# Kernel optimization log

Hardware: AMD Instinct MI355X
Metric: run time of the kernel (lower is better)

## Reference

```python
import jax, jax.numpy as jnp
import numpy as np

N, E = 100000, 1600000
IN_C, HID, OUT_C = 128, 16, 32
H1, H2 = 8, 8  # heads for conv1/conv2; conv3 has 1 head, concat=False
NEG_SLOPE = 0.2


def setup_inputs() -> dict:
    key = jax.random.key(0)
    ks = jax.random.split(key, 16)
    def p(k, shape, fan_in):
        return jax.random.normal(k, shape, jnp.float32) * (1.0 / np.sqrt(fan_in))
    inp = {
        "x": jax.random.normal(ks[0], (N, IN_C), jnp.float32),
        "edge_index": jax.random.randint(ks[1], (2, E), 0, N, jnp.int32),
        # conv1: in=128 -> heads=8, ch=16, concat
        "W1": p(ks[2], (IN_C, H1 * HID), IN_C),
        "a_src1": p(ks[3], (H1, HID), HID),
        "a_dst1": p(ks[4], (H1, HID), HID),
        "b1": jnp.zeros((H1 * HID,), jnp.float32),
        # conv2: in=128 -> heads=8, ch=16, concat
        "W2": p(ks[5], (H1 * HID, H2 * HID), H1 * HID),
        "a_src2": p(ks[6], (H2, HID), HID),
        "a_dst2": p(ks[7], (H2, HID), HID),
        "b2": jnp.zeros((H2 * HID,), jnp.float32),
        # conv3: in=128 -> heads=1, ch=32, concat=False
        "W3": p(ks[8], (H2 * HID, OUT_C), H2 * HID),
        "a_src3": p(ks[9], (1, OUT_C), OUT_C),
        "a_dst3": p(ks[10], (1, OUT_C), OUT_C),
        "b3": jnp.zeros((OUT_C,), jnp.float32),
    }
    return inp


def gat_conv(x, src, dst, W, a_src, a_dst, b, heads, ch, concat):
    """PyG-style GATConv (eval mode): gather -> leaky_relu -> segment softmax -> scatter sum."""
    n = x.shape[0]
    h = (x @ W).reshape(n, heads, ch)                 # [N, H, C]
    al_s = jnp.sum(h * a_src, axis=-1)                # [N, H] source-side logit part
    al_d = jnp.sum(h * a_dst, axis=-1)                # [N, H] dest-side logit part
    logits = jax.nn.leaky_relu(al_s[src] + al_d[dst], NEG_SLOPE)  # [Etot, H]
    m = jax.ops.segment_max(logits, dst, num_segments=n)         # per-dest max (self loops guarantee >=1 edge)
    e = jnp.exp(logits - m[dst])
    denom = jax.ops.segment_sum(e, dst, num_segments=n)
    alpha = e / denom[dst]                            # [Etot, H]
    msgs = h[src] * alpha[..., None]                  # [Etot, H, C]
    out = jax.ops.segment_sum(msgs, dst, num_segments=n)  # [N, H, C]
    if concat:
        return out.reshape(n, heads * ch) + b
    return out.mean(axis=1) + b


def reference(x, edge_index, W1, a_src1, a_dst1, b1, W2, a_src2, a_dst2, b2,
              W3, a_src3, a_dst3, b3):
    n = x.shape[0]
    loops = jnp.arange(n, dtype=edge_index.dtype)     # PyG add_self_loops=True
    src = jnp.concatenate([edge_index[0], loops])
    dst = jnp.concatenate([edge_index[1], loops])
    h = jax.nn.relu(gat_conv(x, src, dst, W1, a_src1, a_dst1, b1, H1, HID, True))
    h = jax.nn.relu(gat_conv(h, src, dst, W2, a_src2, a_dst2, b2, H2, HID, True))
    h = gat_conv(h, src, dst, W3, a_src3, a_dst3, b3, 1, OUT_C, False)
    # global_mean_pool with all-zero batch vector -> mean over all nodes
    return h.mean(axis=0, keepdims=True)              # [1, OUT_C]
```

## Files before the change

### kernel.cpp

```cpp
#include <hip/hip_runtime.h>


typedef unsigned short bfu;
typedef unsigned char u8;
typedef __attribute__((ext_vector_type(8))) short bf16x8;
typedef __attribute__((ext_vector_type(4))) float f32x4;
typedef __attribute__((ext_vector_type(2))) float f32x2;
typedef __attribute__((ext_vector_type(4))) int i32x4;

constexpr int N_NODES = 100000;
constexpr int E_IN    = 1600000;
constexpr int E_TOT   = E_IN + N_NODES;
constexpr float NEG   = 0.2f;
constexpr int P_XCD   = 8;
constexpr int PSZ     = N_NODES / P_XCD;
constexpr int CAP     = 64;
constexpr int AGG32_B = N_NODES / 32;
constexpr int GEMM_B  = (N_NODES + 63) / 64;
constexpr int FUSE_B  = (N_NODES + 63) / 64;
constexpr int EDGE_B4 = (E_TOT / 4 + 255) / 256;
constexpr int FILL_B  = EDGE_B4 * P_XCD;
constexpr int PREP_ITEMS = 43008;
constexpr int PREP_B  = (PREP_ITEMS + 255) / 256;

__device__ inline bfu f2bf(float f) {
    union { float f; unsigned i; } c; c.f = f;
    unsigned x = c.i;
    return (bfu)((x + 0x7fffu + ((x >> 16) & 1u)) >> 16);
}
__device__ inline u8 f2fp8(float f) {
    return (u8)(__builtin_amdgcn_cvt_pk_fp8_f32(f, f, 0, false) & 0xff);
}


__device__ inline void prep_body(int idx,
        const float* __restrict__ W1, const float* __restrict__ W2,
        const float* __restrict__ W3,
        const float* __restrict__ as1, const float* __restrict__ ad1,
        const float* __restrict__ as2, const float* __restrict__ ad2,
        const float* __restrict__ as3, const float* __restrict__ ad3,
        bfu* __restrict__ WtX1, bfu* __restrict__ WtX2, bfu* __restrict__ WtX3) {
    if (idx < 16384) {
        int k = idx >> 7, n = idx & 127;
        WtX1[n * 128 + k] = f2bf(W1[idx]);
    } else if (idx < 32768) {
        int r = idx - 16384;
        int k = r >> 7, n = r & 127;
        WtX2[n * 128 + k] = f2bf(W2[r]);
    } else if (idx < 36864) {
        int r = idx - 32768;
        int k = r >> 5, n = r & 31;
        WtX3[n * 128 + k] = f2bf(W3[r]);
    } else if (idx < 38912) {
        int r = idx - 36864;
        int sd = r >> 10, rr = r & 1023;
        int h = rr >> 7, k = rr & 127;
        const float* a = sd ? ad1 : as1;
        float v = 0.f;
        #pragma unroll
        for (int c = 0; c < 16; ++c) v += W1[k * 128 + h * 16 + c] * a[h * 16 + c];
        WtX1[(128 + sd * 8 + h) * 128 + k] = f2bf(v);
    } else if (idx < 40960) {
        int r = idx - 38912;
        int sd = r >> 10, rr = r & 1023;
        int h = rr >> 7, k = rr & 127;
        const float* a = sd ? ad2 : as2;
        float v = 0.f;
        #pragma unroll
        for (int c = 0; c < 16; ++c) v += W2[k * 128 + h * 16 + c] * a[h * 16 + c];
        WtX2[(128 + sd * 8 + h) * 128 + k] = f2bf(v);
    } else if (idx < 41216) {
        int r = idx - 40960;
        int sd = r >> 7, k = r & 127;
        const float* a = sd ? ad3 : as3;
        float v = 0.f;
        #pragma unroll
        for (int c = 0; c < 32; ++c) v += W3[k * 32 + c] * a[c];
        WtX3[(32 + sd) * 128 + k] = f2bf(v);
    } else if (idx < 43008) {
        WtX3[34 * 128 + (idx - 41216)] = 0;
    }
}

__global__ __launch_bounds__(256) void prep_cursor(
        const float* __restrict__ W1, const float* __restrict__ W2,
        const float* __restrict__ W3,
        const float* __restrict__ as1, const float* __restrict__ ad1,
        const float* __restrict__ as2, const float* __restrict__ ad2,
        const float* __restrict__ as3, const float* __restrict__ ad3,
        bfu* __restrict__ WtX1, bfu* __restrict__ WtX2, bfu* __restrict__ WtX3,
        int* __restrict__ cursor, float* __restrict__ outp) {
    int idx = blockIdx.x * 256 + threadIdx.x;
    prep_body(idx, W1, W2, W3, as1, ad1, as2, ad2, as3, ad3, WtX1, WtX2, WtX3);
    for (int i = idx; i < N_NODES; i += PREP_ITEMS) cursor[i] = 0;
    if (idx < 32) outp[idx] = 0.f;
}


__global__ __launch_bounds__(256) void fill(const int* __restrict__ ei,
        int* __restrict__ cursor, int* __restrict__ srclist) {
    int p = blockIdx.x & 7;
    int b = blockIdx.x >> 3;
    int lo = p * PSZ, hi = lo + PSZ;
    int e0 = (b * 256 + threadIdx.x) * 4;
    if (e0 >= E_TOT) return;
    bool self = e0 >= E_IN;
    i32x4 d4, s4;
    if (!self) {
        d4 = __builtin_nontemporal_load((const i32x4*)&ei[E_IN + e0]);
        s4 = __builtin_nontemporal_load((const i32x4*)&ei[e0]);
    } else {
        int bb = e0 - E_IN;
        d4[0] = bb; d4[1] = bb + 1; d4[2] = bb + 2; d4[3] = bb + 3;
        s4 = d4;
    }
    int pos[4];
    #pragma unroll
    for (int q = 0; q < 4; ++q) {
        int d = d4[q];
        pos[q] = (d >= lo && d < hi) ? atomicAdd(&cursor[d], 1) : -1;
    }
    #pragma unroll
    for (int q = 0; q < 4; ++q) {
        if (pos[q] >= 0 && pos[q] < CAP)
            srclist[d4[q] * CAP + pos[q]] = s4[q];
    }
}


__device__ inline bf16x8 ldcvt_f32(const float* p) {
    float4 v0 = *(const float4*)p;
    float4 v1 = *(const float4*)(p + 4);
    bf16x8 a;
    a[0] = (short)f2bf(v0.x); a[1] = (short)f2bf(v0.y);
    a[2] = (short)f2bf(v0.z); a[3] = (short)f2bf(v0.w);
    a[4] = (short)f2bf(v1.x); a[5] = (short)f2bf(v1.y);
    a[6] = (short)f2bf(v1.z); a[7] = (short)f2bf(v1.w);
    return a;
}

__global__ __launch_bounds__(256) void gemm_mfma_l1(const float* __restrict__ Xg,
                                                    const bfu* __restrict__ Wt,
                                                    u8* __restrict__ Y,
                                                    float* __restrict__ als,
                                                    float* __restrict__ ald) {
    constexpr int NTO = 8;
    constexpr int COUT = 128;
    int wid  = threadIdx.x >> 6;
    int lane = threadIdx.x & 63;
    int m = lane & 15, quad = lane >> 4;
    int rbase = (blockIdx.x * 4 + wid) * 16;
    if (rbase >= N_NODES) return;
    int rA = rbase + m; if (rA >= N_NODES) rA = N_NODES - 1;

    const float* Ap = Xg + (size_t)rA * 128 + quad * 8;
    bf16x8 a0 = ldcvt_f32(Ap);
    bf16x8 a1 = ldcvt_f32(Ap + 32);
    bf16x8 a2 = ldcvt_f32(Ap + 64);
    bf16x8 a3 = ldcvt_f32(Ap + 96);

    const bfu* Bp = Wt + (size_t)m * 128 + quad * 8;
    f32x4 acc[NTO + 1];
    #pragma unroll
    for (int nt = 0; nt <= NTO; nt++) {
        const bfu* Bn = Bp + nt * 16 * 128;
        f32x4 c = {0.f, 0.f, 0.f, 0.f};
        c = __builtin_amdgcn_mfma_f32_16x16x32_bf16(a0, *(const bf16x8*)(Bn),      c, 0, 0, 0);
        c = __builtin_amdgcn_mfma_f32_16x16x32_bf16(a1, *(const bf16x8*)(Bn + 32), c, 0, 0, 0);
        c = __builtin_amdgcn_mfma_f32_16x16x32_bf16(a2, *(const bf16x8*)(Bn + 64), c, 0, 0, 0);
        c = __builtin_amdgcn_mfma_f32_16x16x32_bf16(a3, *(const bf16x8*)(Bn + 96), c, 0, 0, 0);
        acc[nt] = c;
    }

    #pragma unroll
    for (int nt = 0; nt < NTO; nt++) {
        #pragma unroll
        for (int r = 0; r < 4; r++) {
            int row = rbase + quad * 4 + r;
            if (row < N_NODES)
                Y[(size_t)row * COUT + nt * 16 + m] = f2fp8(acc[nt][r]);
        }
    }
    #pragma unroll
    for (int r = 0; r < 4; r++) {
        int row = rbase + quad * 4 + r;
        if (row >= N_NODES) continue;
        float v = acc[NTO][r];
        if (m < 8) als[row * 8 + m] = v;
        else       ald[row * 8 + (m - 8)] = v;
    }
}


__device__ inline void unpack_fma(uint4 u, float w, float* a) {
    f32x2 p;
    p = __builtin_amdgcn_cvt_pk_f32_fp8((int)u.x, false); a[0]=fmaf(w,p[0],a[0]);  a[1]=fmaf(w,p[1],a[1]);
    p = __builtin_amdgcn_cvt_pk_f32_fp8((int)u.x, true);  a[2]=fmaf(w,p[0],a[2]);  a[3]=fmaf(w,p[1],a[3]);
    p = __builtin_amdgcn_cvt_pk_f32_fp8((int)u.y, false); a[4]=fmaf(w,p[0],a[4]);  a[5]=fmaf(w,p[1],a[5]);
    p = __builtin_amdgcn_cvt_pk_f32_fp8((int)u.y, true);  a[6]=fmaf(w,p[0],a[6]);  a[7]=fmaf(w,p[1],a[7]);
    p = __builtin_amdgcn_cvt_pk_f32_fp8((int)u.z, false); a[8]=fmaf(w,p[0],a[8]);  a[9]=fmaf(w,p[1],a[9]);
    p = __builtin_amdgcn_cvt_pk_f32_fp8((int)u.z, true);  a[10]=fmaf(w,p[0],a[10]); a[11]=fmaf(w,p[1],a[11]);
    p = __builtin_amdgcn_cvt_pk_f32_fp8((int)u.w, false); a[12]=fmaf(w,p[0],a[12]); a[13]=fmaf(w,p[1],a[13]);
    p = __builtin_amdgcn_cvt_pk_f32_fp8((int)u.w, true);  a[14]=fmaf(w,p[0],a[14]); a[15]=fmaf(w,p[1],a[15]);
}

template<int NTO>
__global__ __launch_bounds__(256) void fused_agg_gemm(
        const u8* __restrict__ Hin,
        const float* __restrict__ als_in,
        const float* __restrict__ ald_in,
        const int* __restrict__ deg, const int* __restrict__ srclist,
        const float* __restrict__ bias,
        const bfu* __restrict__ Wt,
        u8* __restrict__ Yout,
        float* __restrict__ als_out, float* __restrict__ ald_out) {
    __shared__ uint4 ldsb[64 * 16];
    int t    = threadIdx.x;
    int wid  = t >> 6;
    int lane = t & 63;
    int sub  = lane >> 3;
    int li   = lane & 7;
    int rbase = blockIdx.x * 64;

    #pragma unroll
    for (int it = 0; it < 2; ++it) {
        int dl = wid * 16 + it * 8 + sub;
        int d  = rbase + dl;
        if (d < N_NODES) {
            int c0 = li * 16;
            float ad = ald_in[d * 8 + li];
            const int* sl = srclist + d * CAP;
            int n = deg[d]; n = n < CAP ? n : CAP;
            float a[16];
            #pragma unroll
            for (int k = 0; k < 16; ++k) a[k] = 0.f;
            float den = 0.f;
            int j = 0;
            for (; j + 2 <= n; j += 2) {
                int s0 = sl[j], s1 = sl[j + 1];
                uint4 u0 = *(const uint4*)(Hin + (size_t)s0 * 128 + c0);
                uint4 u1 = *(const uint4*)(Hin + (size_t)s1 * 128 + c0);
                float x0 = als_in[s0 * 8 + li], x1 = als_in[s1 * 8 + li];
                float l0 = x0 + ad; l0 = fmaxf(l0, NEG * l0); float w0 = __expf(l0);
                float l1 = x1 + ad; l1 = fmaxf(l1, NEG * l1); float w1 = __expf(l1);
                den += w0 + w1;
                unpack_fma(u0, w0, a);
                unpack_fma(u1, w1, a);
            }
            if (j < n) {
                int s0 = sl[j];
                uint4 u0 = *(const uint4*)(Hin + (size_t)s0 * 128 + c0);
                float x0 = als_in[s0 * 8 + li];
                float l0 = x0 + ad; l0 = fmaxf(l0, NEG * l0); float w0 = __expf(l0);
                den += w0;
                unpack_fma(u0, w0, a);
            }
            float r = 1.f / den;
            unsigned dw[8];
            #pragma unroll
            for (int k = 0; k < 8; ++k) {
                float e0 = fmaxf(fmaf(a[2*k],   r, bias[c0 + 2*k]),   0.f);
                float e1 = fmaxf(fmaf(a[2*k+1], r, bias[c0 + 2*k+1]), 0.f);
                dw[k] = (unsigned)f2bf(e0) | ((unsigned)f2bf(e1) << 16);
            }
            uint4 st0 = {dw[0], dw[1], dw[2], dw[3]};
            uint4 st1 = {dw[4], dw[5], dw[6], dw[7]};
            int sw = dl & 7;
            ldsb[dl * 16 + ((li * 2)     ^ sw)] = st0;
            ldsb[dl * 16 + ((li * 2 + 1) ^ sw)] = st1;
        }
    }
    __syncthreads();

    constexpr int COUT = NTO * 16;
    int m = lane & 15, quad = lane >> 4;
    int lr = wid * 16 + m;
    int lb = lr * 16, sw = lr & 7;
    bf16x8 a0 = *(const bf16x8*)&ldsb[lb + ((quad)      ^ sw)];
    bf16x8 a1 = *(const bf16x8*)&ldsb[lb + ((quad + 4)  ^ sw)];
    bf16x8 a2 = *(const bf16x8*)&ldsb[lb + ((quad + 8)  ^ sw)];
    bf16x8 a3 = *(const bf16x8*)&ldsb[lb + ((quad + 12) ^ sw)];

    const bfu* Bp = Wt + (size_t)m * 128 + quad * 8;
    f32x4 acc[NTO + 1];
    #pragma unroll
    for (int nt = 0; nt <= NTO; nt++) {
        const bfu* Bn = Bp + nt * 16 * 128;
        f32x4 c = {0.f, 0.f, 0.f, 0.f};
        c = __builtin_amdgcn_mfma_f32_16x16x32_bf16(a0, *(const bf16x8*)(Bn),      c, 0, 0, 0);
        c = __builtin_amdgcn_mfma_f32_16x16x32_bf16(a1, *(const bf16x8*)(Bn + 32), c, 0, 0, 0);
        c = __builtin_amdgcn_mfma_f32_16x16x32_bf16(a2, *(const bf16x8*)(Bn + 64), c, 0, 0, 0);
        c = __builtin_amdgcn_mfma_f32_16x16x32_bf16(a3, *(const bf16x8*)(Bn + 96), c, 0, 0, 0);
        acc[nt] = c;
    }

    #pragma unroll
    for (int nt = 0; nt < NTO; nt++) {
        #pragma unroll
        for (int r = 0; r < 4; r++) {
            int row = rbase + wid * 16 + quad * 4 + r;
            if (row < N_NODES)
                Yout[(size_t)row * COUT + nt * 16 + m] = f2fp8(acc[nt][r]);
        }
    }
    #pragma unroll
    for (int r = 0; r < 4; r++) {
        int row = rbase + wid * 16 + quad * 4 + r;
        if (row >= N_NODES) continue;
        float v = acc[NTO][r];
        if constexpr (NTO == 8) {
            if (m < 8) als_out[row * 8 + m] = v;
            else       ald_out[row * 8 + (m - 8)] = v;
        } else {
            if (m == 0) als_out[row] = v;
            else if (m == 1) ald_out[row] = v;
        }
    }
}


__global__ __launch_bounds__(256) void agg32(const u8* __restrict__ Hb,
        const float* __restrict__ als, const float* __restrict__ ald,
        const int* __restrict__ deg, const int* __restrict__ srclist,
        const float* __restrict__ bias, float* __restrict__ outp) {
    __shared__ float lds[4][32];
    int t    = threadIdx.x;
    int wid  = t >> 6;
    int lane = t & 63;
    int sub  = lane >> 3;
    int li   = lane & 7;
    int d    = blockIdx.x * 32 + wid * 8 + sub;
    int c0 = li * 4;
    float adv = ald[d];
    const int* sl = srclist + d * CAP;
    int n = deg[d]; n = n < CAP ? n : CAP;
    float a0=0.f,a1=0.f,a2=0.f,a3=0.f,den=0.f;
    int j = 0;
    for (; j + 4 <= n; j += 4) {
        int s0 = sl[j], s1 = sl[j+1], s2 = sl[j+2], s3 = sl[j+3];
        unsigned u0 = *(const unsigned*)(Hb + (size_t)s0 * 32 + c0);
        unsigned u1 = *(const unsigned*)(Hb + (size_t)s1 * 32 + c0);
        unsigned u2 = *(const unsigned*)(Hb + (size_t)s2 * 32 + c0);
        unsigned u3 = *(const unsigned*)(Hb + (size_t)s3 * 32 + c0);
        float x0 = als[s0], x1 = als[s1], x2 = als[s2], x3 = als[s3];
        float l0 = x0 + adv; l0 = fmaxf(l0, NEG*l0); float w0 = __expf(l0);
        float l1 = x1 + adv; l1 = fmaxf(l1, NEG*l1); float w1 = __expf(l1);
        float l2 = x2 + adv; l2 = fmaxf(l2, NEG*l2); float w2 = __expf(l2);
        float l3 = x3 + adv; l3 = fmaxf(l3, NEG*l3); float w3 = __expf(l3);
        den += (w0 + w1) + (w2 + w3);
        f32x2 p;
        p = __builtin_amdgcn_cvt_pk_f32_fp8((int)u0, false); a0=fmaf(w0,p[0],a0); a1=fmaf(w0,p[1],a1);
        p = __builtin_amdgcn_cvt_pk_f32_fp8((int)u0, true);  a2=fmaf(w0,p[0],a2); a3=fmaf(w0,p[1],a3);
        p = __builtin_amdgcn_cvt_pk_f32_fp8((int)u1, false); a0=fmaf(w1,p[0],a0); a1=fmaf(w1,p[1],a1);
        p = __builtin_amdgcn_cvt_pk_f32_fp8((int)u1, true);  a2=fmaf(w1,p[0],a2); a3=fmaf(w1,p[1],a3);
        p = __builtin_amdgcn_cvt_pk_f32_fp8((int)u2, false); a0=fmaf(w2,p[0],a0); a1=fmaf(w2,p[1],a1);
        p = __builtin_amdgcn_cvt_pk_f32_fp8((int)u2, true);  a2=fmaf(w2,p[0],a2); a3=fmaf(w2,p[1],a3);
        p = __builtin_amdgcn_cvt_pk_f32_fp8((int)u3, false); a0=fmaf(w3,p[0],a0); a1=fmaf(w3,p[1],a1);
        p = __builtin_amdgcn_cvt_pk_f32_fp8((int)u3, true);  a2=fmaf(w3,p[0],a2); a3=fmaf(w3,p[1],a3);
    }
    for (; j < n; ++j) {
        int s0 = sl[j];
        unsigned u0 = *(const unsigned*)(Hb + (size_t)s0 * 32 + c0);
        float x0 = als[s0];
        float l0 = x0 + adv; l0 = fmaxf(l0, NEG*l0); float w0 = __expf(l0);
        den += w0;
        f32x2 p;
        p = __builtin_amdgcn_cvt_pk_f32_fp8((int)u0, false); a0=fmaf(w0,p[0],a0); a1=fmaf(w0,p[1],a1);
        p = __builtin_amdgcn_cvt_pk_f32_fp8((int)u0, true);  a2=fmaf(w0,p[0],a2); a3=fmaf(w0,p[1],a3);
    }
    float r = 1.f / den;
    float4 bv = *(const float4*)&bias[c0];
    float o0 = fmaf(a0, r, bv.x), o1 = fmaf(a1, r, bv.y);
    float o2 = fmaf(a2, r, bv.z), o3 = fmaf(a3, r, bv.w);
    #pragma unroll
    for (int mask = 8; mask < 64; mask <<= 1) {
        o0 += __shfl_xor(o0, mask);
        o1 += __shfl_xor(o1, mask);
        o2 += __shfl_xor(o2, mask);
        o3 += __shfl_xor(o3, mask);
    }
    if (sub == 0) {
        lds[wid][c0]     = o0;
        lds[wid][c0 + 1] = o1;
        lds[wid][c0 + 2] = o2;
        lds[wid][c0 + 3] = o3;
    }
    __syncthreads();
    if (t < 32)
        atomicAdd(&outp[t],
            (lds[0][t] + lds[1][t] + lds[2][t] + lds[3][t]) * (1.0f / N_NODES));
}


extern "C" void kernel_launch(void* const* d_in, const int* in_sizes, int n_in,
                              void* d_out, int out_size, void* d_ws, size_t ws_size,
                              hipStream_t stream) {
    (void)in_sizes; (void)n_in; (void)out_size; (void)ws_size;
    const float* x   = (const float*)d_in[0];
    const int*   ei  = (const int*)d_in[1];
    const float* W1  = (const float*)d_in[2];
    const float* as1 = (const float*)d_in[3];
    const float* ad1 = (const float*)d_in[4];
    const float* b1  = (const float*)d_in[5];
    const float* W2  = (const float*)d_in[6];
    const float* as2 = (const float*)d_in[7];
    const float* ad2 = (const float*)d_in[8];
    const float* b2  = (const float*)d_in[9];
    const float* W3  = (const float*)d_in[10];
    const float* as3 = (const float*)d_in[11];
    const float* ad3 = (const float*)d_in[12];
    const float* b3  = (const float*)d_in[13];

    char* ws = (char*)d_ws;
    size_t off = 0;
    auto carve = [&](size_t bytes) { void* p = ws + off; off += (bytes + 255) & ~size_t(255); return p; };
    u8*    bufHa   = (u8*)carve(size_t(N_NODES) * 128);
    u8*    bufHb   = (u8*)carve(size_t(N_NODES) * 128);
    float* alsA    = (float*)carve(size_t(N_NODES) * 8 * 4);
    float* aldA    = (float*)carve(size_t(N_NODES) * 8 * 4);
    float* alsB    = (float*)carve(size_t(N_NODES) * 8 * 4);
    float* aldB    = (float*)carve(size_t(N_NODES) * 8 * 4);
    int*   cursor  = (int*)carve(size_t(N_NODES) * 4);
    bfu*   WtX1    = (bfu*)carve(144 * 128 * 2);
    bfu*   WtX2    = (bfu*)carve(144 * 128 * 2);
    bfu*   WtX3    = (bfu*)carve(48 * 128 * 2);
    int*   srclist = (int*)carve(size_t(N_NODES) * CAP * 4);

    prep_cursor<<<PREP_B, 256, 0, stream>>>(W1, W2, W3,
        as1, ad1, as2, ad2, as3, ad3, WtX1, WtX2, WtX3, cursor, (float*)d_out);

    fill<<<FILL_B, 256, 0, stream>>>(ei, cursor, srclist);

    gemm_mfma_l1<<<GEMM_B, 256, 0, stream>>>(x, WtX1, bufHa, alsA, aldA);

    fused_agg_gemm<8><<<FUSE_B, 256, 0, stream>>>(bufHa, alsA, aldA,
        cursor, srclist, b1, WtX2, bufHb, alsB, aldB);

    fused_agg_gemm<2><<<FUSE_B, 256, 0, stream>>>(bufHb, alsB, aldB,
        cursor, srclist, b2, WtX3, bufHa, alsA, aldA);

    agg32<<<AGG32_B, 256, 0, stream>>>(bufHa, alsA, aldA, cursor, srclist, b3, (float*)d_out);
}
```

Baseline: 430.2 us.

## Bucket adjacency lists by source-node range to improve gather locality

The per-destination source list is split into 8 buckets keyed by source node range, each with its own counter and a capacity of 14. The aggregation kernels walk the buckets in order, so the neighbour-feature gathers are grouped by source partition, which may improve cache locality across XCDs. In exchange there are 8x more counters, more atomics spread over more addresses, smaller unroll, and a cap of 14 per bucket that could drop edges when the source distribution is uneven.

```diff
diff --git a/kernel.cpp b/kernel.cpp
--- a/kernel.cpp
+++ b/kernel.cpp
@@ -14,7 +14,9 @@
 constexpr float NEG   = 0.2f;
 constexpr int P_XCD   = 8;
 constexpr int PSZ     = N_NODES / P_XCD;
-constexpr int CAP     = 64;
+constexpr int NR      = 8;
+constexpr int CAP_R   = 14;
+constexpr int SL_STRIDE = NR * CAP_R;
 constexpr int AGG32_B = N_NODES / 32;
 constexpr int GEMM_B  = (N_NODES + 63) / 64;
 constexpr int FUSE_B  = (N_NODES + 63) / 64;
@@ -92,7 +94,7 @@
         int* __restrict__ cursor, float* __restrict__ outp) {
     int idx = blockIdx.x * 256 + threadIdx.x;
     prep_body(idx, W1, W2, W3, as1, ad1, as2, ad2, as3, ad3, WtX1, WtX2, WtX3);
-    for (int i = idx; i < N_NODES; i += PREP_ITEMS) cursor[i] = 0;
+    for (int i = idx; i < N_NODES * NR; i += PREP_ITEMS) cursor[i] = 0;
     if (idx < 32) outp[idx] = 0.f;
 }
 
@@ -114,16 +116,16 @@
         d4[0] = bb; d4[1] = bb + 1; d4[2] = bb + 2; d4[3] = bb + 3;
         s4 = d4;
     }
-    int pos[4];
     #pragma unroll
     for (int q = 0; q < 4; ++q) {
         int d = d4[q];
-        pos[q] = (d >= lo && d < hi) ? atomicAdd(&cursor[d], 1) : -1;
-    }
-    #pragma unroll
-    for (int q = 0; q < 4; ++q) {
-        if (pos[q] >= 0 && pos[q] < CAP)
-            srclist[d4[q] * CAP + pos[q]] = s4[q];
+        if (d >= lo && d < hi) {
+            int s = s4[q];
+            int r = s / PSZ;
+            int pos = atomicAdd(&cursor[d * NR + r], 1);
+            if (pos < CAP_R)
+                srclist[(size_t)d * SL_STRIDE + r * CAP_R + pos] = s;
+        }
     }
 }
 
@@ -229,31 +231,37 @@
         if (d < N_NODES) {
             int c0 = li * 16;
             float ad = ald_in[d * 8 + li];
-            const int* sl = srclist + d * CAP;
-            int n = deg[d]; n = n < CAP ? n : CAP;
+            const int* sl = srclist + (size_t)d * SL_STRIDE;
+            int cnt[8];
+            *(i32x4*)&cnt[0] = *(const i32x4*)&deg[d * NR];
+            *(i32x4*)&cnt[4] = *(const i32x4*)&deg[d * NR + 4];
             float a[16];
             #pragma unroll
             for (int k = 0; k < 16; ++k) a[k] = 0.f;
             float den = 0.f;
-            int j = 0;
-            for (; j + 2 <= n; j += 2) {
-                int s0 = sl[j], s1 = sl[j + 1];
-                uint4 u0 = *(const uint4*)(Hin + (size_t)s0 * 128 + c0);
-                uint4 u1 = *(const uint4*)(Hin + (size_t)s1 * 128 + c0);
-                float x0 = als_in[s0 * 8 + li], x1 = als_in[s1 * 8 + li];
-                float l0 = x0 + ad; l0 = fmaxf(l0, NEG * l0); float w0 = __expf(l0);
-                float l1 = x1 + ad; l1 = fmaxf(l1, NEG * l1); float w1 = __expf(l1);
-                den += w0 + w1;
-                unpack_fma(u0, w0, a);
-                unpack_fma(u1, w1, a);
-            }
-            if (j < n) {
-                int s0 = sl[j];
-                uint4 u0 = *(const uint4*)(Hin + (size_t)s0 * 128 + c0);
-                float x0 = als_in[s0 * 8 + li];
-                float l0 = x0 + ad; l0 = fmaxf(l0, NEG * l0); float w0 = __expf(l0);
-                den += w0;
-                unpack_fma(u0, w0, a);
+            for (int r = 0; r < NR; ++r) {
+                int n = cnt[r]; n = n < CAP_R ? n : CAP_R;
+                const int* slr = sl + r * CAP_R;
+                int j = 0;
+                for (; j + 2 <= n; j += 2) {
+                    int s0 = slr[j], s1 = slr[j + 1];
+                    uint4 u0 = *(const uint4*)(Hin + (size_t)s0 * 128 + c0);
+                    uint4 u1 = *(const uint4*)(Hin + (size_t)s1 * 128 + c0);
+                    float x0 = als_in[s0 * 8 + li], x1 = als_in[s1 * 8 + li];
+                    float l0 = x0 + ad; l0 = fmaxf(l0, NEG * l0); float w0 = __expf(l0);
+                    float l1 = x1 + ad; l1 = fmaxf(l1, NEG * l1); float w1 = __expf(l1);
+                    den += w0 + w1;
+                    unpack_fma(u0, w0, a);
+                    unpack_fma(u1, w1, a);
+                }
+                if (j < n) {
+                    int s0 = slr[j];
+                    uint4 u0 = *(const uint4*)(Hin + (size_t)s0 * 128 + c0);
+                    float x0 = als_in[s0 * 8 + li];
+                    float l0 = x0 + ad; l0 = fmaxf(l0, NEG * l0); float w0 = __expf(l0);
+                    den += w0;
+                    unpack_fma(u0, w0, a);
+                }
             }
             float r = 1.f / den;
             unsigned dw[8];
@@ -332,41 +340,39 @@
     int d    = blockIdx.x * 32 + wid * 8 + sub;
     int c0 = li * 4;
     float adv = ald[d];
-    const int* sl = srclist + d * CAP;
-    int n = deg[d]; n = n < CAP ? n : CAP;
+    const int* sl = srclist + (size_t)d * SL_STRIDE;
+    int cnt[8];
+    *(i32x4*)&cnt[0] = *(const i32x4*)&deg[d * NR];
+    *(i32x4*)&cnt[4] = *(const i32x4*)&deg[d * NR + 4];
     float a0=0.f,a1=0.f,a2=0.f,a3=0.f,den=0.f;
-    int j = 0;
-    for (; j + 4 <= n; j += 4) {
-        int s0 = sl[j], s1 = sl[j+1], s2 = sl[j+2], s3 = sl[j+3];
-        unsigned u0 = *(const unsigned*)(Hb + (size_t)s0 * 32 + c0);
-        unsigned u1 = *(const unsigned*)(Hb + (size_t)s1 * 32 + c0);
-        unsigned u2 = *(const unsigned*)(Hb + (size_t)s2 * 32 + c0);
-        unsigned u3 = *(const unsigned*)(Hb + (size_t)s3 * 32 + c0);
-        float x0 = als[s0], x1 = als[s1], x2 = als[s2], x3 = als[s3];
-        float l0 = x0 + adv; l0 = fmaxf(l0, NEG*l0); float w0 = __expf(l0);
-        float l1 = x1 + adv; l1 = fmaxf(l1, NEG*l1); float w1 = __expf(l1);
-        float l2 = x2 + adv; l2 = fmaxf(l2, NEG*l2); float w2 = __expf(l2);
-        float l3 = x3 + adv; l3 = fmaxf(l3, NEG*l3); float w3 = __expf(l3);
-        den += (w0 + w1) + (w2 + w3);
-        f32x2 p;
-        p = __builtin_amdgcn_cvt_pk_f32_fp8((int)u0, false); a0=fmaf(w0,p[0],a0); a1=fmaf(w0,p[1],a1);
-        p = __builtin_amdgcn_cvt_pk_f32_fp8((int)u0, true);  a2=fmaf(w0,p[0],a2); a3=fmaf(w0,p[1],a3);
-        p = __builtin_amdgcn_cvt_pk_f32_fp8((int)u1, false); a0=fmaf(w1,p[0],a0); a1=fmaf(w1,p[1],a1);
-        p = __builtin_amdgcn_cvt_pk_f32_fp8((int)u1, true);  a2=fmaf(w1,p[0],a2); a3=fmaf(w1,p[1],a3);
-        p = __builtin_amdgcn_cvt_pk_f32_fp8((int)u2, false); a0=fmaf(w2,p[0],a0); a1=fmaf(w2,p[1],a1);
-        p = __builtin_amdgcn_cvt_pk_f32_fp8((int)u2, true);  a2=fmaf(w2,p[0],a2); a3=fmaf(w2,p[1],a3);
-        p = __builtin_amdgcn_cvt_pk_f32_fp8((int)u3, false); a0=fmaf(w3,p[0],a0); a1=fmaf(w3,p[1],a1);
-        p = __builtin_amdgcn_cvt_pk_f32_fp8((int)u3, true);  a2=fmaf(w3,p[0],a2); a3=fmaf(w3,p[1],a3);
-    }
-    for (; j < n; ++j) {
-        int s0 = sl[j];
-        unsigned u0 = *(const unsigned*)(Hb + (size_t)s0 * 32 + c0);
-        float x0 = als[s0];
-        float l0 = x0 + adv; l0 = fmaxf(l0, NEG*l0); float w0 = __expf(l0);
-        den += w0;
-        f32x2 p;
-        p = __builtin_amdgcn_cvt_pk_f32_fp8((int)u0, false); a0=fmaf(w0,p[0],a0); a1=fmaf(w0,p[1],a1);
-        p = __builtin_amdgcn_cvt_pk_f32_fp8((int)u0, true);  a2=fmaf(w0,p[0],a2); a3=fmaf(w0,p[1],a3);
+    for (int r = 0; r < NR; ++r) {
+        int n = cnt[r]; n = n < CAP_R ? n : CAP_R;
+        const int* slr = sl + r * CAP_R;
+        int j = 0;
+        for (; j + 2 <= n; j += 2) {
+            int s0 = slr[j], s1 = slr[j+1];
+            unsigned u0 = *(const unsigned*)(Hb + (size_t)s0 * 32 + c0);
+            unsigned u1 = *(const unsigned*)(Hb + (size_t)s1 * 32 + c0);
+            float x0 = als[s0], x1 = als[s1];
+            float l0 = x0 + adv; l0 = fmaxf(l0, NEG*l0); float w0 = __expf(l0);
+            float l1 = x1 + adv; l1 = fmaxf(l1, NEG*l1); float w1 = __expf(l1);
+            den += w0 + w1;
+            f32x2 p;
+            p = __builtin_amdgcn_cvt_pk_f32_fp8((int)u0, false); a0=fmaf(w0,p[0],a0); a1=fmaf(w0,p[1],a1);
+            p = __builtin_amdgcn_cvt_pk_f32_fp8((int)u0, true);  a2=fmaf(w0,p[0],a2); a3=fmaf(w0,p[1],a3);
+            p = __builtin_amdgcn_cvt_pk_f32_fp8((int)u1, false); a0=fmaf(w1,p[0],a0); a1=fmaf(w1,p[1],a1);
+            p = __builtin_amdgcn_cvt_pk_f32_fp8((int)u1, true);  a2=fmaf(w1,p[0],a2); a3=fmaf(w1,p[1],a3);
+        }
+        if (j < n) {
+            int s0 = slr[j];
+            unsigned u0 = *(const unsigned*)(Hb + (size_t)s0 * 32 + c0);
+            float x0 = als[s0];
+            float l0 = x0 + adv; l0 = fmaxf(l0, NEG*l0); float w0 = __expf(l0);
+            den += w0;
+            f32x2 p;
+            p = __builtin_amdgcn_cvt_pk_f32_fp8((int)u0, false); a0=fmaf(w0,p[0],a0); a1=fmaf(w0,p[1],a1);
+            p = __builtin_amdgcn_cvt_pk_f32_fp8((int)u0, true);  a2=fmaf(w0,p[0],a2); a3=fmaf(w0,p[1],a3);
+        }
     }
     float r = 1.f / den;
     float4 bv = *(const float4*)&bias[c0];
@@ -420,11 +426,11 @@
     float* aldA    = (float*)carve(size_t(N_NODES) * 8 * 4);
     float* alsB    = (float*)carve(size_t(N_NODES) * 8 * 4);
     float* aldB    = (float*)carve(size_t(N_NODES) * 8 * 4);
-    int*   cursor  = (int*)carve(size_t(N_NODES) * 4);
+    int*   cursor  = (int*)carve(size_t(N_NODES) * NR * 4);
     bfu*   WtX1    = (bfu*)carve(144 * 128 * 2);
     bfu*   WtX2    = (bfu*)carve(144 * 128 * 2);
     bfu*   WtX3    = (bfu*)carve(48 * 128 * 2);
-    int*   srclist = (int*)carve(size_t(N_NODES) * CAP * 4);
+    int*   srclist = (int*)carve(size_t(N_NODES) * SL_STRIDE * 4);
 
     prep_cursor<<<PREP_B, 256, 0, stream>>>(W1, W2, W3,
         as1, ad1, as2, ad2, as3, ad3, WtX1, WtX2, WtX3, cursor, (float*)d_out);
```

Result: slower. 496.2 us (+15.3%).
